# Kernel optimization log

Measured on AMD Instinct MI355X. Metric: run time of the kernel, lower is better.

The kernel has to match this reference:

```python
import jax, jax.numpy as jnp
import numpy as np

B, S, D, H, E = 4, 2048, 1024, 4096, 8
THRESHOLD = 0.5


def setup_inputs() -> dict:
    key = jax.random.key(0)
    ks = jax.random.split(key, 7)
    s_in = 1.0 / np.sqrt(D)
    s_h = 1.0 / np.sqrt(H)
    return {
        "x": jax.random.normal(ks[0], (B, S, D), dtype=jnp.float32),
        "Wg": jax.random.uniform(ks[1], (D, E), jnp.float32, -s_in, s_in),
        "bg": jax.random.uniform(ks[2], (E,), jnp.float32, -s_in, s_in),
        "W1": jax.random.uniform(ks[3], (E, D, H), jnp.float32, -s_in, s_in),
        "b1": jax.random.uniform(ks[4], (E, H), jnp.float32, -s_in, s_in),
        "W2": jax.random.uniform(ks[5], (E, H, D), jnp.float32, -s_h, s_h),
        "b2": jax.random.uniform(ks[6], (E, D), jnp.float32, -s_h, s_h),
    }


def reference(x, Wg, bg, W1, b1, W2, b2):
    b, s, d = x.shape
    x_flat = x.reshape(-1, d)                       # [T, D], T = B*S
    # Top-any gating: sigmoid logits, threshold mask, weights = probs * mask
    probs = jax.nn.sigmoid(x_flat @ Wg + bg)        # [T, E]
    mask = (probs > THRESHOLD).astype(x_flat.dtype)
    weights = probs * mask                          # [T, E]
    # Dense per-expert MLP over all tokens (faithful to the torch loop)
    h = jax.nn.relu(jnp.einsum('td,edh->eth', x_flat, W1) + b1[:, None, :])  # [E, T, H]
    expert_out = jnp.einsum('eth,ehd->etd', h, W2) + b2[:, None, :]          # [E, T, D]
    combined = jnp.einsum('te,etd->td', weights, expert_out)                 # [T, D]
    return combined.reshape(b, s, d)
```

## Files before the change

### kernel.cpp

```cpp
#include <hip/hip_runtime.h>
#include <hip/hip_bf16.h>

#define T_TOK 8192
#define D_DIM 1024
#define H_DIM 4096
#define E_NUM 8
#define IDXST 8448
#define CAPBLK 18
#define CAPROWS (CAPBLK * 256)

typedef short bf16x8 __attribute__((ext_vector_type(8)));
typedef float f32x4 __attribute__((ext_vector_type(4)));

__device__ __forceinline__ unsigned short f2bf(float f) {
    union { float f; unsigned int u; } v; v.f = f;
    unsigned int u = v.u;
    u = u + 0x7FFFu + ((u >> 16) & 1u);
    return (unsigned short)(u >> 16);
}

__device__ __forceinline__ void gload_lds16(const void* g, void* l) {
    __builtin_amdgcn_global_load_lds(
        (const __attribute__((address_space(1))) unsigned int*)g,
        (__attribute__((address_space(3))) unsigned int*)l,
        16, 0, 0);
}

#define SBAR() { __builtin_amdgcn_sched_barrier(0); __builtin_amdgcn_s_barrier(); __builtin_amdgcn_sched_barrier(0); }
#define LGKM0() { asm volatile("s_waitcnt lgkmcnt(0)" ::: "memory"); __builtin_amdgcn_sched_barrier(0); }
#define VMC4() { asm volatile("s_waitcnt vmcnt(4)" ::: "memory"); __builtin_amdgcn_sched_barrier(0); }
#define VMC6() { asm volatile("s_waitcnt vmcnt(6)" ::: "memory"); __builtin_amdgcn_sched_barrier(0); }
#define VMC0() { asm volatile("s_waitcnt vmcnt(0)" ::: "memory"); __builtin_amdgcn_sched_barrier(0); }

__device__ __forceinline__ void swz_bmbn(int lin, int nbm, int nbn, int& bm, int& bn) {
    const int nwg = nbm * nbn;
    int wgid = ((nwg & 7) == 0) ? ((lin & 7) * (nwg >> 3) + (lin >> 3)) : lin;
    if ((nbm & 7) == 0 && (nbn & 3) == 0) {
        const int per = nbn << 3;
        int stripe = wgid / per;
        int l = wgid - stripe * per;
        int g = l >> 5, r = l & 31;
        bm = stripe * 8 + (r >> 2);
        bn = g * 4 + (r & 3);
    } else {
        bm = wgid / nbn;
        bn = wgid - bm * nbn;
    }
}

__device__ __forceinline__ int swz_rt(int lin, int n) {
    int q = n >> 3, r = n & 7;
    int xcd = lin & 7, pos = lin >> 3;
    int base = (xcd < r) ? xcd * (q + 1) : r * (q + 1) + (xcd - r) * q;
    return base + pos;
}

template<int NBN>
__device__ __forceinline__ bool merged_map(const int* __restrict__ cntp,
                                           int& e, int& bm, int& bn, int& cnt_e) {
    int nbs[E_NUM], tot = 0;
    #pragma unroll
    for (int i = 0; i < E_NUM; ++i) {
        int c = cntp[i];
        int nbm = (c + 255) >> 8;
        if (nbm > CAPBLK) nbm = CAPBLK;
        nbs[i] = nbm * NBN;
        tot += nbs[i];
    }
    if ((int)blockIdx.x >= tot) return false;
    const int wg = swz_rt(blockIdx.x, tot);
    int acc = 0, loc = 0;
    e = 0;
    #pragma unroll
    for (int i = 0; i < E_NUM; ++i) {
        if (wg >= acc && wg < acc + nbs[i]) { e = i; loc = wg - acc; }
        acc += nbs[i];
    }
    bm = loc / NBN;
    bn = loc - bm * NBN;
    cnt_e = cntp[e];
    return true;
}

__global__ void gate_cvt_kernel(const float* __restrict__ x, const float* __restrict__ Wg,
                                const float* __restrict__ bg, float* __restrict__ wout,
                                unsigned short* __restrict__ xb) {
    int wv = (int)((blockIdx.x * blockDim.x + threadIdx.x) >> 6);
    int lane = threadIdx.x & 63;
    if (wv >= T_TOK) return;
    const float* xr = x + (size_t)wv * D_DIM;
    unsigned short* xo = xb + (size_t)wv * D_DIM;
    double acc[E_NUM] = {0, 0, 0, 0, 0, 0, 0, 0};
    for (int i = 0; i < D_DIM / 64; ++i) {
        int d = i * 64 + lane;
        float xf = xr[d];
        xo[d] = f2bf(xf);
        double xv = (double)xf;
        const float* wr = Wg + (size_t)d * E_NUM;
        #pragma unroll
        for (int e = 0; e < E_NUM; ++e) acc[e] += xv * (double)wr[e];
    }
    #pragma unroll
    for (int e = 0; e < E_NUM; ++e) {
        double v = acc[e];
        for (int s = 32; s; s >>= 1) v += __shfl_down(v, s, 64);
        acc[e] = v;
    }
    if (lane == 0) {
        #pragma unroll
        for (int e = 0; e < E_NUM; ++e) {
            double z = acc[e] + (double)bg[e];
            float p = (float)(1.0 / (1.0 + exp(-z)));
            wout[(size_t)wv * E_NUM + e] = (p > 0.5f) ? p : 0.0f;
        }
    }
}

__global__ void compact_kernel(const float* __restrict__ wgt, int* __restrict__ idx,
                               float* __restrict__ wc, int* __restrict__ cnt) {
    const int e = blockIdx.x;
    const int tid = threadIdx.x;
    const int lane = tid & 63, wv = tid >> 6;
    int* idxe = idx + e * IDXST;
    float* wce = wc + e * IDXST;
    __shared__ int wtot[4];
    __shared__ int sbase;
    if (tid == 0) sbase = 0;
    __syncthreads();
    for (int t0 = 0; t0 < T_TOK; t0 += 256) {
        int t = t0 + tid;
        float w = wgt[(size_t)t * E_NUM + e];
        int act = (w > 0.0f) ? 1 : 0;
        unsigned long long mask = __ballot(act);
        int wpos = __popcll(mask & ((1ull << lane) - 1ull));
        if (lane == 0) wtot[wv] = __popcll(mask);
        __syncthreads();
        int off = sbase;
        for (int i = 0; i < wv; ++i) off += wtot[i];
        if (act) { idxe[off + wpos] = t; wce[off + wpos] = w; }
        __syncthreads();
        if (tid == 0) sbase += wtot[0] + wtot[1] + wtot[2] + wtot[3];
        __syncthreads();
    }
    int total = sbase;
    int padded = ((total + 255) / 256) * 256;
    for (int i = total + tid; i < padded; i += 256) { idxe[i] = 0; wce[i] = 0.0f; }
    if (tid == 0) cnt[e] = total;
}

__global__ void transpose_cvt(const float* __restrict__ in, unsigned short* __restrict__ out,
                              int R, int C) {
    __shared__ unsigned short tile[64][65];
    int e = blockIdx.z;
    const float* src = in + (size_t)e * R * C;
    unsigned short* dst = out + (size_t)e * R * C;
    int c0 = blockIdx.x * 64, r0 = blockIdx.y * 64;
    int t = threadIdx.x;
    int cc = (t & 15) * 4;
    int rr = t >> 4;
    #pragma unroll
    for (int p = 0; p < 4; ++p) {
        int r = rr + p * 16;
        float4 v = *(const float4*)(src + (size_t)(r0 + r) * C + c0 + cc);
        tile[cc + 0][r] = f2bf(v.x);
        tile[cc + 1][r] = f2bf(v.y);
        tile[cc + 2][r] = f2bf(v.z);
        tile[cc + 3][r] = f2bf(v.w);
    }
    __syncthreads();
    int rr4 = (t & 15) * 4;
    int cw = t >> 4;
    #pragma unroll
    for (int p = 0; p < 4; ++p) {
        int c = cw + p * 16;
        ushort4 o;
        o.x = tile[c][rr4 + 0];
        o.y = tile[c][rr4 + 1];
        o.z = tile[c][rr4 + 2];
        o.w = tile[c][rr4 + 3];
        *(ushort4*)(dst + (size_t)(c0 + c) * R + r0 + rr4) = o;
    }
}

__global__ void zero_kernel(float4* __restrict__ p, size_t n4) {
    size_t i = (size_t)blockIdx.x * blockDim.x + threadIdx.x;
    size_t st = (size_t)gridDim.x * blockDim.x;
    for (; i < n4; i += st) p[i] = (float4){0.f, 0.f, 0.f, 0.f};
}

__global__ void sentinel_kernel(float* out, size_t n) {
    size_t i = (size_t)blockIdx.x * blockDim.x + threadIdx.x;
    size_t st = (size_t)gridDim.x * blockDim.x;
    for (; i < n; i += st) out[i] = 12345.0f;
}

__global__ __launch_bounds__(512, 2) void gemm1c(
    const unsigned short* __restrict__ Xb,
    const unsigned short* __restrict__ W1T,
    unsigned short* __restrict__ Hc,
    const float* __restrict__ b1,
    const int* __restrict__ idxb,
    const float* __restrict__ wcb,
    const int* __restrict__ cntp)
{
    __shared__ __align__(16) unsigned short lA[2][16384];
    __shared__ __align__(16) unsigned short lB[2][16384];

    int e, bm, bn, cnt;
    if (!merged_map<H_DIM / 256>(cntp, e, bm, bn, cnt)) return;

    const int* idx = idxb + e * IDXST;
    const float* wc = wcb + e * IDXST;
    const unsigned short* Bmat = W1T + (size_t)e * H_DIM * D_DIM;
    const float* b1e = b1 + (size_t)e * H_DIM;
    unsigned short* HcE = Hc + (size_t)e * CAPROWS * H_DIM;

    const int tid = threadIdx.x;
    const int lane = tid & 63, wid = tid >> 6;
    const int wr = wid >> 2;
    const int wcn = wid & 3;
    const int fr = lane & 15, fq = lane >> 4;

    const int srow = tid >> 3;
    const int scol = (((tid & 7) ^ (srow & 7)) << 3);

    const unsigned short* Asrc[4];
    #pragma unroll
    for (int h = 0; h < 4; ++h)
        Asrc[h] = Xb + (size_t)idx[bm * 256 + h * 64 + srow] * D_DIM + scol;
    const unsigned short* Bb = Bmat + (size_t)(bn * 256 + srow) * D_DIM + scol;

    const int s0 = ((0 << 2) | fq) ^ (fr & 7);
    const int s1 = ((1 << 2) | fq) ^ (fr & 7);

    f32x4 acc[8][4];
    #pragma unroll
    for (int m = 0; m < 8; ++m)
        #pragma unroll
        for (int n = 0; n < 4; ++n)
            acc[m][n] = (f32x4){0.f, 0.f, 0.f, 0.f};

    bf16x8 a[4][2], b[4][2];

    auto stageA = [&](int bf, int hf, int kt) {
        gload_lds16(Asrc[hf * 2]     + kt * 64, &lA[bf][hf * 8192 + tid * 8]);
        gload_lds16(Asrc[hf * 2 + 1] + kt * 64, &lA[bf][hf * 8192 + 4096 + tid * 8]);
    };
    auto stageB = [&](int bf, int hf, int kt) {
        const unsigned short* s = Bb + (size_t)(hf * 128) * D_DIM + kt * 64;
        gload_lds16(s,                      &lB[bf][hf * 8192 + tid * 8]);
        gload_lds16(s + (size_t)64 * D_DIM, &lB[bf][hf * 8192 + 4096 + tid * 8]);
    };

    stageB(0, 0, 0);
    stageA(0, 0, 0);
    stageA(0, 1, 0);
    stageB(0, 1, 0);
    stageB(1, 0, 1);
    stageA(1, 0, 1);
    VMC4();
    SBAR();

    int cur = 0;
    for (int t = 0; t < 16; ++t) {
        const int nxt = cur ^ 1;
        #pragma unroll
        for (int mm = 0; mm < 4; ++mm) {
            const int r = wr * 128 + mm * 16 + fr;
            a[mm][0] = *(const bf16x8*)&lA[cur][r * 64 + s0 * 8];
            a[mm][1] = *(const bf16x8*)&lA[cur][r * 64 + s1 * 8];
        }
        #pragma unroll
        for (int n = 0; n < 2; ++n) {
            const int r = wcn * 64 + n * 16 + fr;
            b[n][0] = *(const bf16x8*)&lB[cur][r * 64 + s0 * 8];
            b[n][1] = *(const bf16x8*)&lB[cur][r * 64 + s1 * 8];
        }
        if (t + 1 < 16) stageA(nxt, 1, t + 1);
        SBAR(); LGKM0();
        __builtin_amdgcn_s_setprio(1);
        #pragma unroll
        for (int kk = 0; kk < 2; ++kk)
            #pragma unroll
            for (int mm = 0; mm < 4; ++mm) {
                acc[mm][0] = __builtin_amdgcn_mfma_f32_16x16x32_bf16(a[mm][kk], b[0][kk], acc[mm][0], 0, 0, 0);
                acc[mm][1] = __builtin_amdgcn_mfma_f32_16x16x32_bf16(a[mm][kk], b[1][kk], acc[mm][1], 0, 0, 0);
            }
        __builtin_amdgcn_s_setprio(0);
        SBAR();
        #pragma unroll
        for (int n = 2; n < 4; ++n) {
            const int r = wcn * 64 + n * 16 + fr;
            b[n][0] = *(const bf16x8*)&lB[cur][r * 64 + s0 * 8];
            b[n][1] = *(const bf16x8*)&lB[cur][r * 64 + s1 * 8];
        }
        if (t + 1 < 16) stageB(nxt, 1, t + 1);
        SBAR(); LGKM0();
        __builtin_amdgcn_s_setprio(1);
        #pragma unroll
        for (int kk = 0; kk < 2; ++kk)
            #pragma unroll
            for (int mm = 0; mm < 4; ++mm) {
                acc[mm][2] = __builtin_amdgcn_mfma_f32_16x16x32_bf16(a[mm][kk], b[2][kk], acc[mm][2], 0, 0, 0);
                acc[mm][3] = __builtin_amdgcn_mfma_f32_16x16x32_bf16(a[mm][kk], b[3][kk], acc[mm][3], 0, 0, 0);
            }
        __builtin_amdgcn_s_setprio(0);
        SBAR();
        #pragma unroll
        for (int mm = 0; mm < 4; ++mm) {
            const int r = wr * 128 + (mm + 4) * 16 + fr;
            a[mm][0] = *(const bf16x8*)&lA[cur][r * 64 + s0 * 8];
            a[mm][1] = *(const bf16x8*)&lA[cur][r * 64 + s1 * 8];
        }
        if (t + 2 < 16) stageB(cur, 0, t + 2);
        SBAR(); LGKM0();
        __builtin_amdgcn_s_setprio(1);
        #pragma unroll
        for (int kk = 0; kk < 2; ++kk)
            #pragma unroll
            for (int mm = 0; mm < 4; ++mm) {
                acc[mm + 4][0] = __builtin_amdgcn_mfma_f32_16x16x32_bf16(a[mm][kk], b[0][kk], acc[mm + 4][0], 0, 0, 0);
                acc[mm + 4][1] = __builtin_amdgcn_mfma_f32_16x16x32_bf16(a[mm][kk], b[1][kk], acc[mm + 4][1], 0, 0, 0);
            }
        __builtin_amdgcn_s_setprio(0);
        SBAR();
        if (t + 2 < 16) stageA(cur, 0, t + 2);
        if (t < 14) { VMC4(); } else { VMC0(); }
        SBAR(); LGKM0();
        __builtin_amdgcn_s_setprio(1);
        #pragma unroll
        for (int kk = 0; kk < 2; ++kk)
            #pragma unroll
            for (int mm = 0; mm < 4; ++mm) {
                acc[mm + 4][2] = __builtin_amdgcn_mfma_f32_16x16x32_bf16(a[mm][kk], b[2][kk], acc[mm + 4][2], 0, 0, 0);
                acc[mm + 4][3] = __builtin_amdgcn_mfma_f32_16x16x32_bf16(a[mm][kk], b[3][kk], acc[mm + 4][3], 0, 0, 0);
            }
        __builtin_amdgcn_s_setprio(0);
        SBAR();
        cur = nxt;
    }

    #pragma unroll
    for (int m = 0; m < 8; ++m) {
        const int rbase = bm * 256 + wr * 128 + m * 16 + fq * 4;
        #pragma unroll
        for (int n = 0; n < 4; ++n) {
            const int cn = bn * 256 + wcn * 64 + n * 16 + fr;
            const float bb = b1e[cn];
            #pragma unroll
            for (int j = 0; j < 4; ++j) {
                const int r = rbase + j;
                const float w = wc[r];
                float v = fmaxf(acc[m][n][j] + bb, 0.0f) * w;
                HcE[(size_t)r * H_DIM + cn] = f2bf(v);
            }
        }
    }
}

__global__ __launch_bounds__(512, 2) void gemm2c(
    const unsigned short* __restrict__ Hc,
    const unsigned short* __restrict__ W2T,
    float* __restrict__ out,
    const float* __restrict__ b2,
    const int* __restrict__ idxb,
    const float* __restrict__ wcb,
    const int* __restrict__ cntp)
{
    __shared__ __align__(16) unsigned short lA[3][16384];
    __shared__ __align__(16) unsigned short lB[3][8192];

    int e, bm, bn, cnt;
    if (!merged_map<D_DIM / 128>(cntp, e, bm, bn, cnt)) return;

    const int* idx = idxb + e * IDXST;
    const float* wc = wcb + e * IDXST;
    const unsigned short* A = Hc + (size_t)e * CAPROWS * H_DIM;
    const unsigned short* Bmat = W2T + (size_t)e * D_DIM * H_DIM;
    const float* b2e = b2 + (size_t)e * D_DIM;

    const int tid = threadIdx.x;
    const int lane = tid & 63, wid = tid >> 6;
    const int wr = wid >> 1;
    const int wcn = wid & 1;
    const int fr = lane & 15, fq = lane >> 4;

    const int srow = tid >> 3;
    const int scol = (((tid & 7) ^ (srow & 7)) << 3);
    const unsigned short* Ab = A + (size_t)(bm * 256 + srow) * H_DIM + scol;
    const unsigned short* Bb = Bmat + (size_t)(bn * 128 + srow) * H_DIM + scol;

    const int s0 = ((0 << 2) | fq) ^ (fr & 7);
    const int s1 = ((1 << 2) | fq) ^ (fr & 7);

    f32x4 acc[4][4];
    #pragma unroll
    for (int m = 0; m < 4; ++m)
        #pragma unroll
        for (int n = 0; n < 4; ++n)
            acc[m][n] = (f32x4){0.f, 0.f, 0.f, 0.f};

    bf16x8 a[4][2], b[4][2];

    auto stageA = [&](int bf, int hf, int kt) {
        const unsigned short* s = Ab + (size_t)(hf * 128) * H_DIM + kt * 64;
        gload_lds16(s,                      &lA[bf][hf * 8192 + tid * 8]);
        gload_lds16(s + (size_t)64 * H_DIM, &lA[bf][hf * 8192 + 4096 + tid * 8]);
    };
    auto stageB = [&](int bf, int kt) {
        const unsigned short* s = Bb + kt * 64;
        gload_lds16(s,                      &lB[bf][tid * 8]);
        gload_lds16(s + (size_t)64 * H_DIM, &lB[bf][4096 + tid * 8]);
    };

    stageA(0, 0, 0); stageA(0, 1, 0); stageB(0, 0);
    stageA(1, 0, 1); stageA(1, 1, 1); stageB(1, 1);
    VMC6();
    SBAR();

    int bt = 0, bs = 2;
    const int NT = H_DIM / 64;
    for (int t = 0; t < NT; ++t) {
        #pragma unroll
        for (int mm = 0; mm < 4; ++mm) {
            const int r = wr * 64 + mm * 16 + fr;
            a[mm][0] = *(const bf16x8*)&lA[bt][r * 64 + s0 * 8];
            a[mm][1] = *(const bf16x8*)&lA[bt][r * 64 + s1 * 8];
        }
        #pragma unroll
        for (int n = 0; n < 2; ++n) {
            const int r = wcn * 64 + n * 16 + fr;
            b[n][0] = *(const bf16x8*)&lB[bt][r * 64 + s0 * 8];
            b[n][1] = *(const bf16x8*)&lB[bt][r * 64 + s1 * 8];
        }
        if (t + 2 < NT) { stageA(bs, 1, t + 2); stageB(bs, t + 2); }
        SBAR(); LGKM0();
        __builtin_amdgcn_s_setprio(1);
        #pragma unroll
        for (int kk = 0; kk < 2; ++kk)
            #pragma unroll
            for (int mm = 0; mm < 4; ++mm) {
                acc[mm][0] = __builtin_amdgcn_mfma_f32_16x16x32_bf16(a[mm][kk], b[0][kk], acc[mm][0], 0, 0, 0);
                acc[mm][1] = __builtin_amdgcn_mfma_f32_16x16x32_bf16(a[mm][kk], b[1][kk], acc[mm][1], 0, 0, 0);
            }
        __builtin_amdgcn_s_setprio(0);
        SBAR();
        #pragma unroll
        for (int n = 2; n < 4; ++n) {
            const int r = wcn * 64 + n * 16 + fr;
            b[n][0] = *(const bf16x8*)&lB[bt][r * 64 + s0 * 8];
            b[n][1] = *(const bf16x8*)&lB[bt][r * 64 + s1 * 8];
        }
        if (t + 2 < NT) { stageA(bs, 0, t + 2); VMC6(); } else { VMC0(); }
        SBAR(); LGKM0();
        __builtin_amdgcn_s_setprio(1);
        #pragma unroll
        for (int kk = 0; kk < 2; ++kk)
            #pragma unroll
            for (int mm = 0; mm < 4; ++mm) {
                acc[mm][2] = __builtin_amdgcn_mfma_f32_16x16x32_bf16(a[mm][kk], b[2][kk], acc[mm][2], 0, 0, 0);
                acc[mm][3] = __builtin_amdgcn_mfma_f32_16x16x32_bf16(a[mm][kk], b[3][kk], acc[mm][3], 0, 0, 0);
            }
        __builtin_amdgcn_s_setprio(0);
        SBAR();
        bt = (bt == 2) ? 0 : bt + 1;
        bs = (bs == 2) ? 0 : bs + 1;
    }

    #pragma unroll
    for (int m = 0; m < 4; ++m) {
        const int rbase = bm * 256 + wr * 64 + m * 16 + fq * 4;
        #pragma unroll
        for (int n = 0; n < 4; ++n) {
            const int cn = bn * 128 + wcn * 64 + n * 16 + fr;
            const float bb = b2e[cn];
            #pragma unroll
            for (int j = 0; j < 4; ++j) {
                const int row = rbase + j;
                if (row < cnt) {
                    const int tok = idx[row];
                    atomicAdd(&out[(size_t)tok * D_DIM + cn], acc[m][n][j] + wc[row] * bb);
                }
            }
        }
    }
}

__global__ __launch_bounds__(512, 2) void gemm1_8ph(
    const unsigned short* __restrict__ A,
    const unsigned short* __restrict__ W1T,
    unsigned short* __restrict__ Hc,
    const float* __restrict__ b1,
    const float* __restrict__ wgt,
    int t0, int e, int nbm)
{
    __shared__ __align__(16) unsigned short lA[2][16384];
    __shared__ __align__(16) unsigned short lB[2][16384];
    const int nbn = H_DIM / 256;
    int bm, bn;
    swz_bmbn(blockIdx.x, nbm, nbn, bm, bn);
    const int tid = threadIdx.x;
    const int lane = tid & 63, wid = tid >> 6;
    const int wr = wid >> 2;
    const int wcn = wid & 3;
    const int fr = lane & 15, fq = lane >> 4;
    const int srow = tid >> 3;
    const int scol = (((tid & 7) ^ (srow & 7)) << 3);
    const unsigned short* Ab = A + (size_t)(bm * 256 + srow) * D_DIM + scol;
    const unsigned short* Bb = W1T + (size_t)e * H_DIM * D_DIM
                             + (size_t)(bn * 256 + srow) * D_DIM + scol;
    const int s0 = ((0 << 2) | fq) ^ (fr & 7);
    const int s1 = ((1 << 2) | fq) ^ (fr & 7);
    f32x4 acc[8][4];
    #pragma unroll
    for (int m = 0; m < 8; ++m)
        #pragma unroll
        for (int n = 0; n < 4; ++n)
            acc[m][n] = (f32x4){0.f, 0.f, 0.f, 0.f};
    bf16x8 a[4][2], b[4][2];
    auto stageA = [&](int bf, int hf, int kt) {
        const unsigned short* s = Ab + (size_t)(hf * 128) * D_DIM + kt * 64;
        gload_lds16(s,                      &lA[bf][hf * 8192 + tid * 8]);
        gload_lds16(s + (size_t)64 * D_DIM, &lA[bf][hf * 8192 + 4096 + tid * 8]);
    };
    auto stageB = [&](int bf, int hf, int kt) {
        const unsigned short* s = Bb + (size_t)(hf * 128) * D_DIM + kt * 64;
        gload_lds16(s,                      &lB[bf][hf * 8192 + tid * 8]);
        gload_lds16(s + (size_t)64 * D_DIM, &lB[bf][hf * 8192 + 4096 + tid * 8]);
    };
    stageB(0, 0, 0); stageA(0, 0, 0); stageA(0, 1, 0); stageB(0, 1, 0);
    stageB(1, 0, 1); stageA(1, 0, 1);
    VMC4();
    SBAR();
    int cur = 0;
    for (int t = 0; t < 16; ++t) {
        const int nxt = cur ^ 1;
        #pragma unroll
        for (int mm = 0; mm < 4; ++mm) {
            const int r = wr * 128 + mm * 16 + fr;
            a[mm][0] = *(const bf16x8*)&lA[cur][r * 64 + s0 * 8];
            a[mm][1] = *(const bf16x8*)&lA[cur][r * 64 + s1 * 8];
        }
        #pragma unroll
        for (int n = 0; n < 2; ++n) {
            const int r = wcn * 64 + n * 16 + fr;
            b[n][0] = *(const bf16x8*)&lB[cur][r * 64 + s0 * 8];
            b[n][1] = *(const bf16x8*)&lB[cur][r * 64 + s1 * 8];
        }
        if (t + 1 < 16) stageA(nxt, 1, t + 1);
        SBAR(); LGKM0();
        __builtin_amdgcn_s_setprio(1);
        #pragma unroll
        for (int kk = 0; kk < 2; ++kk)
            #pragma unroll
            for (int mm = 0; mm < 4; ++mm) {
                acc[mm][0] = __builtin_amdgcn_mfma_f32_16x16x32_bf16(a[mm][kk], b[0][kk], acc[mm][0], 0, 0, 0);
                acc[mm][1] = __builtin_amdgcn_mfma_f32_16x16x32_bf16(a[mm][kk], b[1][kk], acc[mm][1], 0, 0, 0);
            }
        __builtin_amdgcn_s_setprio(0);
        SBAR();
        #pragma unroll
        for (int n = 2; n < 4; ++n) {
            const int r = wcn * 64 + n * 16 + fr;
            b[n][0] = *(const bf16x8*)&lB[cur][r * 64 + s0 * 8];
            b[n][1] = *(const bf16x8*)&lB[cur][r * 64 + s1 * 8];
        }
        if (t + 1 < 16) stageB(nxt, 1, t + 1);
        SBAR(); LGKM0();
        __builtin_amdgcn_s_setprio(1);
        #pragma unroll
        for (int kk = 0; kk < 2; ++kk)
            #pragma unroll
            for (int mm = 0; mm < 4; ++mm) {
                acc[mm][2] = __builtin_amdgcn_mfma_f32_16x16x32_bf16(a[mm][kk], b[2][kk], acc[mm][2], 0, 0, 0);
                acc[mm][3] = __builtin_amdgcn_mfma_f32_16x16x32_bf16(a[mm][kk], b[3][kk], acc[mm][3], 0, 0, 0);
            }
        __builtin_amdgcn_s_setprio(0);
        SBAR();
        #pragma unroll
        for (int mm = 0; mm < 4; ++mm) {
            const int r = wr * 128 + (mm + 4) * 16 + fr;
            a[mm][0] = *(const bf16x8*)&lA[cur][r * 64 + s0 * 8];
            a[mm][1] = *(const bf16x8*)&lA[cur][r * 64 + s1 * 8];
        }
        if (t + 2 < 16) stageB(cur, 0, t + 2);
        SBAR(); LGKM0();
        __builtin_amdgcn_s_setprio(1);
        #pragma unroll
        for (int kk = 0; kk < 2; ++kk)
            #pragma unroll
            for (int mm = 0; mm < 4; ++mm) {
                acc[mm + 4][0] = __builtin_amdgcn_mfma_f32_16x16x32_bf16(a[mm][kk], b[0][kk], acc[mm + 4][0], 0, 0, 0);
                acc[mm + 4][1] = __builtin_amdgcn_mfma_f32_16x16x32_bf16(a[mm][kk], b[1][kk], acc[mm + 4][1], 0, 0, 0);
            }
        __builtin_amdgcn_s_setprio(0);
        SBAR();
        if (t + 2 < 16) stageA(cur, 0, t + 2);
        if (t < 14) { VMC4(); } else { VMC0(); }
        SBAR(); LGKM0();
        __builtin_amdgcn_s_setprio(1);
        #pragma unroll
        for (int kk = 0; kk < 2; ++kk)
            #pragma unroll
            for (int mm = 0; mm < 4; ++mm) {
                acc[mm + 4][2] = __builtin_amdgcn_mfma_f32_16x16x32_bf16(a[mm][kk], b[2][kk], acc[mm + 4][2], 0, 0, 0);
                acc[mm + 4][3] = __builtin_amdgcn_mfma_f32_16x16x32_bf16(a[mm][kk], b[3][kk], acc[mm + 4][3], 0, 0, 0);
            }
        __builtin_amdgcn_s_setprio(0);
        SBAR();
        cur = nxt;
    }
    #pragma unroll
    for (int m = 0; m < 8; ++m) {
        const int rbase = bm * 256 + wr * 128 + m * 16 + fq * 4;
        #pragma unroll
        for (int n = 0; n < 4; ++n) {
            const int cn = bn * 256 + wcn * 64 + n * 16 + fr;
            const float bb = b1[(size_t)e * H_DIM + cn];
            #pragma unroll
            for (int j = 0; j < 4; ++j) {
                const int r = rbase + j;
                const float w = wgt[(size_t)(t0 + r) * E_NUM + e];
                float v = fmaxf(acc[m][n][j] + bb, 0.0f) * w;
                Hc[(size_t)r * H_DIM + cn] = f2bf(v);
            }
        }
    }
}

template<int MODE>
__global__ __launch_bounds__(512, 2) void gemm2_8ph(
    const unsigned short* __restrict__ A,
    const unsigned short* __restrict__ B,
    float* __restrict__ out,
    const float* __restrict__ bias,
    const float* __restrict__ wts,
    int t0, int e, int nbm)
{
    __shared__ __align__(16) unsigned short lA[3][16384];
    __shared__ __align__(16) unsigned short lB[3][8192];
    const int nbn = D_DIM / 128;
    int bm, bn;
    swz_bmbn(blockIdx.x, nbm, nbn, bm, bn);
    const int tid = threadIdx.x;
    const int lane = tid & 63, wid = tid >> 6;
    const int wr = wid >> 1;
    const int wcn = wid & 1;
    const int fr = lane & 15, fq = lane >> 4;
    const int srow = tid >> 3;
    const int scol = (((tid & 7) ^ (srow & 7)) << 3);
    const unsigned short* Ab = A + (size_t)(bm * 256 + srow) * H_DIM + scol;
    const unsigned short* Bb = B + (size_t)(bn * 128 + srow) * H_DIM + scol;
    const int s0 = ((0 << 2) | fq) ^ (fr & 7);
    const int s1 = ((1 << 2) | fq) ^ (fr & 7);
    f32x4 acc[4][4];
    #pragma unroll
    for (int m = 0; m < 4; ++m)
        #pragma unroll
        for (int n = 0; n < 4; ++n)
            acc[m][n] = (f32x4){0.f, 0.f, 0.f, 0.f};
    bf16x8 a[4][2], b[4][2];
    auto stageA = [&](int bf, int hf, int kt) {
        const unsigned short* s = Ab + (size_t)(hf * 128) * H_DIM + kt * 64;
        gload_lds16(s,                      &lA[bf][hf * 8192 + tid * 8]);
        gload_lds16(s + (size_t)64 * H_DIM, &lA[bf][hf * 8192 + 4096 + tid * 8]);
    };
    auto stageB = [&](int bf, int kt) {
        const unsigned short* s = Bb + kt * 64;
        gload_lds16(s,                      &lB[bf][tid * 8]);
        gload_lds16(s + (size_t)64 * H_DIM, &lB[bf][4096 + tid * 8]);
    };
    stageA(0, 0, 0); stageA(0, 1, 0); stageB(0, 0);
    stageA(1, 0, 1); stageA(1, 1, 1); stageB(1, 1);
    VMC6();
    SBAR();
    int bt = 0, bs = 2;
    const int NT = H_DIM / 64;
    for (int t = 0; t < NT; ++t) {
        #pragma unroll
        for (int mm = 0; mm < 4; ++mm) {
            const int r = wr * 64 + mm * 16 + fr;
            a[mm][0] = *(const bf16x8*)&lA[bt][r * 64 + s0 * 8];
            a[mm][1] = *(const bf16x8*)&lA[bt][r * 64 + s1 * 8];
        }
        #pragma unroll
        for (int n = 0; n < 2; ++n) {
            const int r = wcn * 64 + n * 16 + fr;
            b[n][0] = *(const bf16x8*)&lB[bt][r * 64 + s0 * 8];
            b[n][1] = *(const bf16x8*)&lB[bt][r * 64 + s1 * 8];
        }
        if (t + 2 < NT) { stageA(bs, 1, t + 2); stageB(bs, t + 2); }
        SBAR(); LGKM0();
        __builtin_amdgcn_s_setprio(1);
        #pragma unroll
        for (int kk = 0; kk < 2; ++kk)
            #pragma unroll
            for (int mm = 0; mm < 4; ++mm) {
                acc[mm][0] = __builtin_amdgcn_mfma_f32_16x16x32_bf16(a[mm][kk], b[0][kk], acc[mm][0], 0, 0, 0);
                acc[mm][1] = __builtin_amdgcn_mfma_f32_16x16x32_bf16(a[mm][kk], b[1][kk], acc[mm][1], 0, 0, 0);
            }
        __builtin_amdgcn_s_setprio(0);
        SBAR();
        #pragma unroll
        for (int n = 2; n < 4; ++n) {
            const int r = wcn * 64 + n * 16 + fr;
            b[n][0] = *(const bf16x8*)&lB[bt][r * 64 + s0 * 8];
            b[n][1] = *(const bf16x8*)&lB[bt][r * 64 + s1 * 8];
        }
        if (t + 2 < NT) { stageA(bs, 0, t + 2); VMC6(); } else { VMC0(); }
        SBAR(); LGKM0();
        __builtin_amdgcn_s_setprio(1);
        #pragma unroll
        for (int kk = 0; kk < 2; ++kk)
            #pragma unroll
            for (int mm = 0; mm < 4; ++mm) {
                acc[mm][2] = __builtin_amdgcn_mfma_f32_16x16x32_bf16(a[mm][kk], b[2][kk], acc[mm][2], 0, 0, 0);
                acc[mm][3] = __builtin_amdgcn_mfma_f32_16x16x32_bf16(a[mm][kk], b[3][kk], acc[mm][3], 0, 0, 0);
            }
        __builtin_amdgcn_s_setprio(0);
        SBAR();
        bt = (bt == 2) ? 0 : bt + 1;
        bs = (bs == 2) ? 0 : bs + 1;
    }
    #pragma unroll
    for (int m = 0; m < 4; ++m) {
        const int rbase = bm * 256 + wr * 64 + m * 16 + fq * 4;
        #pragma unroll
        for (int n = 0; n < 4; ++n) {
            const int cn = bn * 128 + wcn * 64 + n * 16 + fr;
            const float bb = bias[cn];
            #pragma unroll
            for (int j = 0; j < 4; ++j) {
                const int row = t0 + rbase + j;
                const float w = wts[(size_t)row * E_NUM + e];
                const float v = acc[m][n][j] + w * bb;
                float* p = out + (size_t)row * D_DIM + cn;
                if (MODE == 1) *p = v;
                else *p += v;
            }
        }
    }
}

extern "C" void kernel_launch(void* const* d_in, const int* in_sizes, int n_in,
                              void* d_out, int out_size, void* d_ws, size_t ws_size,
                              hipStream_t stream) {
    const float* x  = (const float*)d_in[0];
    const float* Wg = (const float*)d_in[1];
    const float* bg = (const float*)d_in[2];
    const float* W1 = (const float*)d_in[3];
    const float* b1 = (const float*)d_in[4];
    const float* W2 = (const float*)d_in[5];
    const float* b2 = (const float*)d_in[6];
    float* out = (float*)d_out;
    char* ws = (char*)d_ws;

    const size_t off_w   = 0;
    const size_t off_idx = 262144;
    const size_t off_wcc = 557056;
    const size_t off_cnt = 851968;
    const size_t off_x   = 1048576;
    const size_t off_w1  = off_x + (size_t)T_TOK * D_DIM * 2;
    const size_t off_w2  = off_w1 + (size_t)E_NUM * D_DIM * H_DIM * 2;
    const size_t off_h   = off_w2 + (size_t)E_NUM * D_DIM * H_DIM * 2;
    const size_t cap_h   = (size_t)E_NUM * CAPROWS * H_DIM * 2;
    const size_t min_h   = (size_t)256 * H_DIM * 2;

    if (ws_size < off_h + min_h) {
        sentinel_kernel<<<2048, 256, 0, stream>>>(out, (size_t)T_TOK * D_DIM);
        return;
    }

    float* wgt = (float*)(ws + off_w);
    int* idxb  = (int*)(ws + off_idx);
    float* wcb = (float*)(ws + off_wcc);
    int* cntb  = (int*)(ws + off_cnt);
    unsigned short* Xb  = (unsigned short*)(ws + off_x);
    unsigned short* W1T = (unsigned short*)(ws + off_w1);
    unsigned short* W2T = (unsigned short*)(ws + off_w2);
    unsigned short* Hc  = (unsigned short*)(ws + off_h);

    gate_cvt_kernel<<<T_TOK / 4, 256, 0, stream>>>(x, Wg, bg, wgt, Xb);
    transpose_cvt<<<dim3(H_DIM / 64, D_DIM / 64, E_NUM), 256, 0, stream>>>(W1, W1T, D_DIM, H_DIM);
    transpose_cvt<<<dim3(D_DIM / 64, H_DIM / 64, E_NUM), 256, 0, stream>>>(W2, W2T, H_DIM, D_DIM);

    if (ws_size >= off_h + cap_h) {
        compact_kernel<<<E_NUM, 256, 0, stream>>>(wgt, idxb, wcb, cntb);
        zero_kernel<<<2048, 256, 0, stream>>>((float4*)out, (size_t)T_TOK * D_DIM / 4);
        const int g1 = E_NUM * CAPBLK * (H_DIM / 256);
        const int g2 = E_NUM * CAPBLK * (D_DIM / 128);
        gemm1c<<<g1, 512, 0, stream>>>(Xb, W1T, Hc, b1, idxb, wcb, cntb);
        gemm2c<<<g2, 512, 0, stream>>>(Hc, W2T, out, b2, idxb, wcb, cntb);
    } else {
        size_t avail = ws_size - off_h;
        size_t tc = avail / ((size_t)H_DIM * 2);
        tc = (tc / 256) * 256;
        if (tc > T_TOK) tc = T_TOK;
        const int TC = (int)tc;
        for (int t0 = 0; t0 < T_TOK; t0 += TC) {
            int cs = (T_TOK - t0 < TC) ? (T_TOK - t0) : TC;
            const int nbm = cs / 256;
            for (int e = 0; e < E_NUM; ++e) {
                gemm1_8ph<<<nbm * (H_DIM / 256), 512, 0, stream>>>(
                    Xb + (size_t)t0 * D_DIM, W1T, Hc, b1, wgt, t0, e, nbm);
                if (e == 0)
                    gemm2_8ph<1><<<nbm * (D_DIM / 128), 512, 0, stream>>>(
                        Hc, W2T + (size_t)e * D_DIM * H_DIM, out,
                        b2 + (size_t)e * D_DIM, wgt, t0, e, nbm);
                else
                    gemm2_8ph<2><<<nbm * (D_DIM / 128), 512, 0, stream>>>(
                        Hc, W2T + (size_t)e * D_DIM * H_DIM, out,
                        b2 + (size_t)e * D_DIM, wgt, t0, e, nbm);
            }
        }
    }
}
```

Baseline: 1.055 ms.

## Split compacted expert GEMM pair into two row-block chunks for cache locality

Runs gemm1c then gemm2c twice, each time over half of every expert's capacity row blocks (blocks 0-8, then 9-17), instead of one large launch of each. The intended gain is that the intermediate H activations written by gemm1 for a chunk are more likely to still be in cache when gemm2 reads them. In exchange it adds two extra kernel launches, shrinks each grid, which can leave a wave tail with idle CUs, and reloads the expert weights once per chunk.

```diff
diff --git a/kernel.cpp b/kernel.cpp
--- a/kernel.cpp
+++ b/kernel.cpp
@@ -7,6 +7,7 @@
 #define E_NUM 8
 #define IDXST 8448
 #define CAPBLK 18
+#define CHALF 9
 #define CAPROWS (CAPBLK * 256)
 
 typedef short bf16x8 __attribute__((ext_vector_type(8)));
@@ -56,18 +57,21 @@
 }
 
 template<int NBN>
-__device__ __forceinline__ bool merged_map(const int* __restrict__ cntp,
+__device__ __forceinline__ bool merged_map(const int* __restrict__ cntp, int chunk,
                                            int& e, int& bm, int& bn, int& cnt_e) {
+    const int lo = chunk ? CHALF : 0;
     int nbs[E_NUM], tot = 0;
     #pragma unroll
     for (int i = 0; i < E_NUM; ++i) {
         int c = cntp[i];
         int nbm = (c + 255) >> 8;
         if (nbm > CAPBLK) nbm = CAPBLK;
-        nbs[i] = nbm * NBN;
+        int hi = chunk ? nbm : ((nbm < CHALF) ? nbm : CHALF);
+        int nb = hi - lo;
+        nbs[i] = (nb > 0) ? nb * NBN : 0;
         tot += nbs[i];
     }
-    if ((int)blockIdx.x >= tot) return false;
+    if (tot == 0 || (int)blockIdx.x >= tot) return false;
     const int wg = swz_rt(blockIdx.x, tot);
     int acc = 0, loc = 0;
     e = 0;
@@ -76,8 +80,8 @@
         if (wg >= acc && wg < acc + nbs[i]) { e = i; loc = wg - acc; }
         acc += nbs[i];
     }
-    bm = loc / NBN;
-    bn = loc - bm * NBN;
+    bm = loc / NBN + lo;
+    bn = loc - (loc / NBN) * NBN;
     cnt_e = cntp[e];
     return true;
 }
@@ -201,13 +205,14 @@
     const float* __restrict__ b1,
     const int* __restrict__ idxb,
     const float* __restrict__ wcb,
-    const int* __restrict__ cntp)
+    const int* __restrict__ cntp,
+    int chunk)
 {
     __shared__ __align__(16) unsigned short lA[2][16384];
     __shared__ __align__(16) unsigned short lB[2][16384];
 
     int e, bm, bn, cnt;
-    if (!merged_map<H_DIM / 256>(cntp, e, bm, bn, cnt)) return;
+    if (!merged_map<H_DIM / 256>(cntp, chunk, e, bm, bn, cnt)) return;
 
     const int* idx = idxb + e * IDXST;
     const float* wc = wcb + e * IDXST;
@@ -365,13 +370,14 @@
     const float* __restrict__ b2,
     const int* __restrict__ idxb,
     const float* __restrict__ wcb,
-    const int* __restrict__ cntp)
+    const int* __restrict__ cntp,
+    int chunk)
 {
     __shared__ __align__(16) unsigned short lA[3][16384];
     __shared__ __align__(16) unsigned short lB[3][8192];
 
     int e, bm, bn, cnt;
-    if (!merged_map<D_DIM / 128>(cntp, e, bm, bn, cnt)) return;
+    if (!merged_map<D_DIM / 128>(cntp, chunk, e, bm, bn, cnt)) return;
 
     const int* idx = idxb + e * IDXST;
     const float* wc = wcb + e * IDXST;
@@ -787,10 +793,12 @@
     if (ws_size >= off_h + cap_h) {
         compact_kernel<<<E_NUM, 256, 0, stream>>>(wgt, idxb, wcb, cntb);
         zero_kernel<<<2048, 256, 0, stream>>>((float4*)out, (size_t)T_TOK * D_DIM / 4);
-        const int g1 = E_NUM * CAPBLK * (H_DIM / 256);
-        const int g2 = E_NUM * CAPBLK * (D_DIM / 128);
-        gemm1c<<<g1, 512, 0, stream>>>(Xb, W1T, Hc, b1, idxb, wcb, cntb);
-        gemm2c<<<g2, 512, 0, stream>>>(Hc, W2T, out, b2, idxb, wcb, cntb);
+        const int g1 = E_NUM * CHALF * (H_DIM / 256);
+        const int g2 = E_NUM * CHALF * (D_DIM / 128);
+        for (int c = 0; c < 2; ++c) {
+            gemm1c<<<g1, 512, 0, stream>>>(Xb, W1T, Hc, b1, idxb, wcb, cntb, c);
+            gemm2c<<<g2, 512, 0, stream>>>(Hc, W2T, out, b2, idxb, wcb, cntb, c);
+        }
     } else {
         size_t avail = ws_size - off_h;
         size_t tc = avail / ((size_t)H_DIM * 2);
```

New measurement: 1.068 ms. Within noise of the previous version (+1.2%).

## Enlarge gemm2c tile to 256x256 with double-buffered 8-phase pipeline

Applied to the files above, without the earlier changes.

Changes the second expert GEMM from 256x128 output tiles with a triple-buffered schedule to 256x256 tiles. It reuses the double-buffered, four-stage MFMA/load interleave already used in gemm1c, with a 2x4 wave layout and 8x4 accumulators per wave. This doubles the reuse of each staged A/B chunk and halves the grid. In exchange it adds accumulator register pressure and gives fewer workgroups, which can leave CUs underfilled when expert token counts are small.

```diff
diff --git a/kernel.cpp b/kernel.cpp
--- a/kernel.cpp
+++ b/kernel.cpp
@@ -29,7 +29,6 @@
 #define SBAR() { __builtin_amdgcn_sched_barrier(0); __builtin_amdgcn_s_barrier(); __builtin_amdgcn_sched_barrier(0); }
 #define LGKM0() { asm volatile("s_waitcnt lgkmcnt(0)" ::: "memory"); __builtin_amdgcn_sched_barrier(0); }
 #define VMC4() { asm volatile("s_waitcnt vmcnt(4)" ::: "memory"); __builtin_amdgcn_sched_barrier(0); }
-#define VMC6() { asm volatile("s_waitcnt vmcnt(6)" ::: "memory"); __builtin_amdgcn_sched_barrier(0); }
 #define VMC0() { asm volatile("s_waitcnt vmcnt(0)" ::: "memory"); __builtin_amdgcn_sched_barrier(0); }
 
 __device__ __forceinline__ void swz_bmbn(int lin, int nbm, int nbn, int& bm, int& bn) {
@@ -262,7 +261,8 @@
     SBAR();
 
     int cur = 0;
-    for (int t = 0; t < 16; ++t) {
+    const int NT = D_DIM / 64;
+    for (int t = 0; t < NT; ++t) {
         const int nxt = cur ^ 1;
         #pragma unroll
         for (int mm = 0; mm < 4; ++mm) {
@@ -276,7 +276,7 @@
             b[n][0] = *(const bf16x8*)&lB[cur][r * 64 + s0 * 8];
             b[n][1] = *(const bf16x8*)&lB[cur][r * 64 + s1 * 8];
         }
-        if (t + 1 < 16) stageA(nxt, 1, t + 1);
+        if (t + 1 < NT) stageA(nxt, 1, t + 1);
         SBAR(); LGKM0();
         __builtin_amdgcn_s_setprio(1);
         #pragma unroll
@@ -294,7 +294,7 @@
             b[n][0] = *(const bf16x8*)&lB[cur][r * 64 + s0 * 8];
             b[n][1] = *(const bf16x8*)&lB[cur][r * 64 + s1 * 8];
         }
-        if (t + 1 < 16) stageB(nxt, 1, t + 1);
+        if (t + 1 < NT) stageB(nxt, 1, t + 1);
         SBAR(); LGKM0();
         __builtin_amdgcn_s_setprio(1);
         #pragma unroll
@@ -312,7 +312,7 @@
             a[mm][0] = *(const bf16x8*)&lA[cur][r * 64 + s0 * 8];
             a[mm][1] = *(const bf16x8*)&lA[cur][r * 64 + s1 * 8];
         }
-        if (t + 2 < 16) stageB(cur, 0, t + 2);
+        if (t + 2 < NT) stageB(cur, 0, t + 2);
         SBAR(); LGKM0();
         __builtin_amdgcn_s_setprio(1);
         #pragma unroll
@@ -324,8 +324,8 @@
             }
         __builtin_amdgcn_s_setprio(0);
         SBAR();
-        if (t + 2 < 16) stageA(cur, 0, t + 2);
-        if (t < 14) { VMC4(); } else { VMC0(); }
+        if (t + 2 < NT) stageA(cur, 0, t + 2);
+        if (t < NT - 2) { VMC4(); } else { VMC0(); }
         SBAR(); LGKM0();
         __builtin_amdgcn_s_setprio(1);
         #pragma unroll
@@ -367,11 +367,11 @@
     const float* __restrict__ wcb,
     const int* __restrict__ cntp)
 {
-    __shared__ __align__(16) unsigned short lA[3][16384];
-    __shared__ __align__(16) unsigned short lB[3][8192];
+    __shared__ __align__(16) unsigned short lA[2][16384];
+    __shared__ __align__(16) unsigned short lB[2][16384];
 
     int e, bm, bn, cnt;
-    if (!merged_map<D_DIM / 128>(cntp, e, bm, bn, cnt)) return;
+    if (!merged_map<D_DIM / 256>(cntp, e, bm, bn, cnt)) return;
 
     const int* idx = idxb + e * IDXST;
     const float* wc = wcb + e * IDXST;
@@ -381,21 +381,21 @@
 
     const int tid = threadIdx.x;
     const int lane = tid & 63, wid = tid >> 6;
-    const int wr = wid >> 1;
-    const int wcn = wid & 1;
+    const int wr = wid >> 2;
+    const int wcn = wid & 3;
     const int fr = lane & 15, fq = lane >> 4;
 
     const int srow = tid >> 3;
     const int scol = (((tid & 7) ^ (srow & 7)) << 3);
     const unsigned short* Ab = A + (size_t)(bm * 256 + srow) * H_DIM + scol;
-    const unsigned short* Bb = Bmat + (size_t)(bn * 128 + srow) * H_DIM + scol;
+    const unsigned short* Bb = Bmat + (size_t)(bn * 256 + srow) * H_DIM + scol;
 
     const int s0 = ((0 << 2) | fq) ^ (fr & 7);
     const int s1 = ((1 << 2) | fq) ^ (fr & 7);
 
-    f32x4 acc[4][4];
-    #pragma unroll
-    for (int m = 0; m < 4; ++m)
+    f32x4 acc[8][4];
+    #pragma unroll
+    for (int m = 0; m < 8; ++m)
         #pragma unroll
         for (int n = 0; n < 4; ++n)
             acc[m][n] = (f32x4){0.f, 0.f, 0.f, 0.f};
@@ -407,33 +407,38 @@
         gload_lds16(s,                      &lA[bf][hf * 8192 + tid * 8]);
         gload_lds16(s + (size_t)64 * H_DIM, &lA[bf][hf * 8192 + 4096 + tid * 8]);
     };
-    auto stageB = [&](int bf, int kt) {
-        const unsigned short* s = Bb + kt * 64;
-        gload_lds16(s,                      &lB[bf][tid * 8]);
-        gload_lds16(s + (size_t)64 * H_DIM, &lB[bf][4096 + tid * 8]);
+    auto stageB = [&](int bf, int hf, int kt) {
+        const unsigned short* s = Bb + (size_t)(hf * 128) * H_DIM + kt * 64;
+        gload_lds16(s,                      &lB[bf][hf * 8192 + tid * 8]);
+        gload_lds16(s + (size_t)64 * H_DIM, &lB[bf][hf * 8192 + 4096 + tid * 8]);
     };
 
-    stageA(0, 0, 0); stageA(0, 1, 0); stageB(0, 0);
-    stageA(1, 0, 1); stageA(1, 1, 1); stageB(1, 1);
-    VMC6();
+    stageB(0, 0, 0);
+    stageA(0, 0, 0);
+    stageA(0, 1, 0);
+    stageB(0, 1, 0);
+    stageB(1, 0, 1);
+    stageA(1, 0, 1);
+    VMC4();
     SBAR();
 
-    int bt = 0, bs = 2;
+    int cur = 0;
     const int NT = H_DIM / 64;
     for (int t = 0; t < NT; ++t) {
+        const int nxt = cur ^ 1;
         #pragma unroll
         for (int mm = 0; mm < 4; ++mm) {
-            const int r = wr * 64 + mm * 16 + fr;
-            a[mm][0] = *(const bf16x8*)&lA[bt][r * 64 + s0 * 8];
-            a[mm][1] = *(const bf16x8*)&lA[bt][r * 64 + s1 * 8];
+            const int r = wr * 128 + mm * 16 + fr;
+            a[mm][0] = *(const bf16x8*)&lA[cur][r * 64 + s0 * 8];
+            a[mm][1] = *(const bf16x8*)&lA[cur][r * 64 + s1 * 8];
         }
         #pragma unroll
         for (int n = 0; n < 2; ++n) {
             const int r = wcn * 64 + n * 16 + fr;
-            b[n][0] = *(const bf16x8*)&lB[bt][r * 64 + s0 * 8];
-            b[n][1] = *(const bf16x8*)&lB[bt][r * 64 + s1 * 8];
-        }
-        if (t + 2 < NT) { stageA(bs, 1, t + 2); stageB(bs, t + 2); }
+            b[n][0] = *(const bf16x8*)&lB[cur][r * 64 + s0 * 8];
+            b[n][1] = *(const bf16x8*)&lB[cur][r * 64 + s1 * 8];
+        }
+        if (t + 1 < NT) stageA(nxt, 1, t + 1);
         SBAR(); LGKM0();
         __builtin_amdgcn_s_setprio(1);
         #pragma unroll
@@ -448,10 +453,10 @@
         #pragma unroll
         for (int n = 2; n < 4; ++n) {
             const int r = wcn * 64 + n * 16 + fr;
-            b[n][0] = *(const bf16x8*)&lB[bt][r * 64 + s0 * 8];
-            b[n][1] = *(const bf16x8*)&lB[bt][r * 64 + s1 * 8];
-        }
-        if (t + 2 < NT) { stageA(bs, 0, t + 2); VMC6(); } else { VMC0(); }
+            b[n][0] = *(const bf16x8*)&lB[cur][r * 64 + s0 * 8];
+            b[n][1] = *(const bf16x8*)&lB[cur][r * 64 + s1 * 8];
+        }
+        if (t + 1 < NT) stageB(nxt, 1, t + 1);
         SBAR(); LGKM0();
         __builtin_amdgcn_s_setprio(1);
         #pragma unroll
@@ -463,16 +468,46 @@
             }
         __builtin_amdgcn_s_setprio(0);
         SBAR();
-        bt = (bt == 2) ? 0 : bt + 1;
-        bs = (bs == 2) ? 0 : bs + 1;
-    }
-
-    #pragma unroll
-    for (int m = 0; m < 4; ++m) {
-        const int rbase = bm * 256 + wr * 64 + m * 16 + fq * 4;
+        #pragma unroll
+        for (int mm = 0; mm < 4; ++mm) {
+            const int r = wr * 128 + (mm + 4) * 16 + fr;
+            a[mm][0] = *(const bf16x8*)&lA[cur][r * 64 + s0 * 8];
+            a[mm][1] = *(const bf16x8*)&lA[cur][r * 64 + s1 * 8];
+        }
+        if (t + 2 < NT) stageB(cur, 0, t + 2);
+        SBAR(); LGKM0();
+        __builtin_amdgcn_s_setprio(1);
+        #pragma unroll
+        for (int kk = 0; kk < 2; ++kk)
+            #pragma unroll
+            for (int mm = 0; mm < 4; ++mm) {
+                acc[mm + 4][0] = __builtin_amdgcn_mfma_f32_16x16x32_bf16(a[mm][kk], b[0][kk], acc[mm + 4][0], 0, 0, 0);
+                acc[mm + 4][1] = __builtin_amdgcn_mfma_f32_16x16x32_bf16(a[mm][kk], b[1][kk], acc[mm + 4][1], 0, 0, 0);
+            }
+        __builtin_amdgcn_s_setprio(0);
+        SBAR();
+        if (t + 2 < NT) stageA(cur, 0, t + 2);
+        if (t < NT - 2) { VMC4(); } else { VMC0(); }
+        SBAR(); LGKM0();
+        __builtin_amdgcn_s_setprio(1);
+        #pragma unroll
+        for (int kk = 0; kk < 2; ++kk)
+            #pragma unroll
+            for (int mm = 0; mm < 4; ++mm) {
+                acc[mm + 4][2] = __builtin_amdgcn_mfma_f32_16x16x32_bf16(a[mm][kk], b[2][kk], acc[mm + 4][2], 0, 0, 0);
+                acc[mm + 4][3] = __builtin_amdgcn_mfma_f32_16x16x32_bf16(a[mm][kk], b[3][kk], acc[mm + 4][3], 0, 0, 0);
+            }
+        __builtin_amdgcn_s_setprio(0);
+        SBAR();
+        cur = nxt;
+    }
+
+    #pragma unroll
+    for (int m = 0; m < 8; ++m) {
+        const int rbase = bm * 256 + wr * 128 + m * 16 + fq * 4;
         #pragma unroll
         for (int n = 0; n < 4; ++n) {
-            const int cn = bn * 128 + wcn * 64 + n * 16 + fr;
+            const int cn = bn * 256 + wcn * 64 + n * 16 + fr;
             const float bb = b2e[cn];
             #pragma unroll
             for (int j = 0; j < 4; ++j) {
@@ -672,7 +707,7 @@
     };
     stageA(0, 0, 0); stageA(0, 1, 0); stageB(0, 0);
     stageA(1, 0, 1); stageA(1, 1, 1); stageB(1, 1);
-    VMC6();
+    asm volatile("s_waitcnt vmcnt(6)" ::: "memory"); __builtin_amdgcn_sched_barrier(0);
     SBAR();
     int bt = 0, bs = 2;
     const int NT = H_DIM / 64;
@@ -707,7 +742,7 @@
             b[n][0] = *(const bf16x8*)&lB[bt][r * 64 + s0 * 8];
             b[n][1] = *(const bf16x8*)&lB[bt][r * 64 + s1 * 8];
         }
-        if (t + 2 < NT) { stageA(bs, 0, t + 2); VMC6(); } else { VMC0(); }
+        if (t + 2 < NT) { stageA(bs, 0, t + 2); asm volatile("s_waitcnt vmcnt(6)" ::: "memory"); __builtin_amdgcn_sched_barrier(0); } else { VMC0(); }
         SBAR(); LGKM0();
         __builtin_amdgcn_s_setprio(1);
         #pragma unroll
@@ -788,7 +823,7 @@
         compact_kernel<<<E_NUM, 256, 0, stream>>>(wgt, idxb, wcb, cntb);
         zero_kernel<<<2048, 256, 0, stream>>>((float4*)out, (size_t)T_TOK * D_DIM / 4);
         const int g1 = E_NUM * CAPBLK * (H_DIM / 256);
-        const int g2 = E_NUM * CAPBLK * (D_DIM / 128);
+        const int g2 = E_NUM * CAPBLK * (D_DIM / 256);
         gemm1c<<<g1, 512, 0, stream>>>(Xb, W1T, Hc, b1, idxb, wcb, cntb);
         gemm2c<<<g2, 512, 0, stream>>>(Hc, W2T, out, b2, idxb, wcb, cntb);
     } else {
```

Measured after the change: 1.044 ms. No clear change (-1.0%).

## Halve gemm2c K-tile to 32 to shrink LDS and raise occupancy

Applied to the files above, without the earlier changes.

The second-GEMM kernel now stages K in steps of 32 instead of 64. This halves its triple-buffered LDS footprint, and the launch bound goes from 2 to 4 workgroups per CU. The inner loop collapses to a single MFMA phase per step with a new XOR swizzle for 32-wide rows, and the wait count is adjusted to match. The aim is more concurrent waves to hide memory latency, at the cost of twice as many barriers and iterations and a tighter register budget that may cause spills.

```diff
diff --git a/kernel.cpp b/kernel.cpp
--- a/kernel.cpp
+++ b/kernel.cpp
@@ -28,8 +28,8 @@
 
 #define SBAR() { __builtin_amdgcn_sched_barrier(0); __builtin_amdgcn_s_barrier(); __builtin_amdgcn_sched_barrier(0); }
 #define LGKM0() { asm volatile("s_waitcnt lgkmcnt(0)" ::: "memory"); __builtin_amdgcn_sched_barrier(0); }
+#define VMC3() { asm volatile("s_waitcnt vmcnt(3)" ::: "memory"); __builtin_amdgcn_sched_barrier(0); }
 #define VMC4() { asm volatile("s_waitcnt vmcnt(4)" ::: "memory"); __builtin_amdgcn_sched_barrier(0); }
-#define VMC6() { asm volatile("s_waitcnt vmcnt(6)" ::: "memory"); __builtin_amdgcn_sched_barrier(0); }
 #define VMC0() { asm volatile("s_waitcnt vmcnt(0)" ::: "memory"); __builtin_amdgcn_sched_barrier(0); }
 
 __device__ __forceinline__ void swz_bmbn(int lin, int nbm, int nbn, int& bm, int& bn) {
@@ -262,7 +262,8 @@
     SBAR();
 
     int cur = 0;
-    for (int t = 0; t < 16; ++t) {
+    const int NT = D_DIM / 64;
+    for (int t = 0; t < NT; ++t) {
         const int nxt = cur ^ 1;
         #pragma unroll
         for (int mm = 0; mm < 4; ++mm) {
@@ -276,7 +277,7 @@
             b[n][0] = *(const bf16x8*)&lB[cur][r * 64 + s0 * 8];
             b[n][1] = *(const bf16x8*)&lB[cur][r * 64 + s1 * 8];
         }
-        if (t + 1 < 16) stageA(nxt, 1, t + 1);
+        if (t + 1 < NT) stageA(nxt, 1, t + 1);
         SBAR(); LGKM0();
         __builtin_amdgcn_s_setprio(1);
         #pragma unroll
@@ -294,7 +295,7 @@
             b[n][0] = *(const bf16x8*)&lB[cur][r * 64 + s0 * 8];
             b[n][1] = *(const bf16x8*)&lB[cur][r * 64 + s1 * 8];
         }
-        if (t + 1 < 16) stageB(nxt, 1, t + 1);
+        if (t + 1 < NT) stageB(nxt, 1, t + 1);
         SBAR(); LGKM0();
         __builtin_amdgcn_s_setprio(1);
         #pragma unroll
@@ -312,7 +313,7 @@
             a[mm][0] = *(const bf16x8*)&lA[cur][r * 64 + s0 * 8];
             a[mm][1] = *(const bf16x8*)&lA[cur][r * 64 + s1 * 8];
         }
-        if (t + 2 < 16) stageB(cur, 0, t + 2);
+        if (t + 2 < NT) stageB(cur, 0, t + 2);
         SBAR(); LGKM0();
         __builtin_amdgcn_s_setprio(1);
         #pragma unroll
@@ -324,8 +325,8 @@
             }
         __builtin_amdgcn_s_setprio(0);
         SBAR();
-        if (t + 2 < 16) stageA(cur, 0, t + 2);
-        if (t < 14) { VMC4(); } else { VMC0(); }
+        if (t + 2 < NT) stageA(cur, 0, t + 2);
+        if (t < NT - 2) { VMC4(); } else { VMC0(); }
         SBAR(); LGKM0();
         __builtin_amdgcn_s_setprio(1);
         #pragma unroll
@@ -358,7 +359,7 @@
     }
 }
 
-__global__ __launch_bounds__(512, 2) void gemm2c(
+__global__ __launch_bounds__(512, 4) void gemm2c(
     const unsigned short* __restrict__ Hc,
     const unsigned short* __restrict__ W2T,
     float* __restrict__ out,
@@ -367,8 +368,8 @@
     const float* __restrict__ wcb,
     const int* __restrict__ cntp)
 {
-    __shared__ __align__(16) unsigned short lA[3][16384];
-    __shared__ __align__(16) unsigned short lB[3][8192];
+    __shared__ __align__(16) unsigned short lA[3][8192];
+    __shared__ __align__(16) unsigned short lB[3][4096];
 
     int e, bm, bn, cnt;
     if (!merged_map<D_DIM / 128>(cntp, e, bm, bn, cnt)) return;
@@ -385,13 +386,12 @@
     const int wcn = wid & 1;
     const int fr = lane & 15, fq = lane >> 4;
 
-    const int srow = tid >> 3;
-    const int scol = (((tid & 7) ^ (srow & 7)) << 3);
+    const int srow = tid >> 2;
+    const int scol = (((tid & 3) ^ ((tid >> 3) & 3)) << 3);
     const unsigned short* Ab = A + (size_t)(bm * 256 + srow) * H_DIM + scol;
     const unsigned short* Bb = Bmat + (size_t)(bn * 128 + srow) * H_DIM + scol;
 
-    const int s0 = ((0 << 2) | fq) ^ (fr & 7);
-    const int s1 = ((1 << 2) | fq) ^ (fr & 7);
+    const int soff = (fq ^ ((fr >> 1) & 3)) * 8;
 
     f32x4 acc[4][4];
     #pragma unroll
@@ -400,71 +400,47 @@
         for (int n = 0; n < 4; ++n)
             acc[m][n] = (f32x4){0.f, 0.f, 0.f, 0.f};
 
-    bf16x8 a[4][2], b[4][2];
-
-    auto stageA = [&](int bf, int hf, int kt) {
-        const unsigned short* s = Ab + (size_t)(hf * 128) * H_DIM + kt * 64;
-        gload_lds16(s,                      &lA[bf][hf * 8192 + tid * 8]);
-        gload_lds16(s + (size_t)64 * H_DIM, &lA[bf][hf * 8192 + 4096 + tid * 8]);
+    bf16x8 a[4], b[4];
+
+    auto stageA = [&](int bf, int kt) {
+        gload_lds16(Ab + kt * 32,                       &lA[bf][tid * 8]);
+        gload_lds16(Ab + (size_t)128 * H_DIM + kt * 32, &lA[bf][4096 + tid * 8]);
     };
     auto stageB = [&](int bf, int kt) {
-        const unsigned short* s = Bb + kt * 64;
-        gload_lds16(s,                      &lB[bf][tid * 8]);
-        gload_lds16(s + (size_t)64 * H_DIM, &lB[bf][4096 + tid * 8]);
+        gload_lds16(Bb + kt * 32, &lB[bf][tid * 8]);
     };
 
-    stageA(0, 0, 0); stageA(0, 1, 0); stageB(0, 0);
-    stageA(1, 0, 1); stageA(1, 1, 1); stageB(1, 1);
-    VMC6();
+    stageA(0, 0); stageB(0, 0);
+    stageA(1, 1); stageB(1, 1);
+    VMC3();
     SBAR();
 
-    int bt = 0, bs = 2;
-    const int NT = H_DIM / 64;
+    const int NT = H_DIM / 32;
+    int cb = 0;
     for (int t = 0; t < NT; ++t) {
+        const int nb2 = (cb + 2 >= 3) ? cb - 1 : cb + 2;
         #pragma unroll
         for (int mm = 0; mm < 4; ++mm) {
             const int r = wr * 64 + mm * 16 + fr;
-            a[mm][0] = *(const bf16x8*)&lA[bt][r * 64 + s0 * 8];
-            a[mm][1] = *(const bf16x8*)&lA[bt][r * 64 + s1 * 8];
-        }
-        #pragma unroll
-        for (int n = 0; n < 2; ++n) {
-            const int r = wcn * 64 + n * 16 + fr;
-            b[n][0] = *(const bf16x8*)&lB[bt][r * 64 + s0 * 8];
-            b[n][1] = *(const bf16x8*)&lB[bt][r * 64 + s1 * 8];
-        }
-        if (t + 2 < NT) { stageA(bs, 1, t + 2); stageB(bs, t + 2); }
-        SBAR(); LGKM0();
-        __builtin_amdgcn_s_setprio(1);
-        #pragma unroll
-        for (int kk = 0; kk < 2; ++kk)
-            #pragma unroll
-            for (int mm = 0; mm < 4; ++mm) {
-                acc[mm][0] = __builtin_amdgcn_mfma_f32_16x16x32_bf16(a[mm][kk], b[0][kk], acc[mm][0], 0, 0, 0);
-                acc[mm][1] = __builtin_amdgcn_mfma_f32_16x16x32_bf16(a[mm][kk], b[1][kk], acc[mm][1], 0, 0, 0);
-            }
-        __builtin_amdgcn_s_setprio(0);
-        SBAR();
-        #pragma unroll
-        for (int n = 2; n < 4; ++n) {
-            const int r = wcn * 64 + n * 16 + fr;
-            b[n][0] = *(const bf16x8*)&lB[bt][r * 64 + s0 * 8];
-            b[n][1] = *(const bf16x8*)&lB[bt][r * 64 + s1 * 8];
-        }
-        if (t + 2 < NT) { stageA(bs, 0, t + 2); VMC6(); } else { VMC0(); }
-        SBAR(); LGKM0();
-        __builtin_amdgcn_s_setprio(1);
-        #pragma unroll
-        for (int kk = 0; kk < 2; ++kk)
-            #pragma unroll
-            for (int mm = 0; mm < 4; ++mm) {
-                acc[mm][2] = __builtin_amdgcn_mfma_f32_16x16x32_bf16(a[mm][kk], b[2][kk], acc[mm][2], 0, 0, 0);
-                acc[mm][3] = __builtin_amdgcn_mfma_f32_16x16x32_bf16(a[mm][kk], b[3][kk], acc[mm][3], 0, 0, 0);
-            }
-        __builtin_amdgcn_s_setprio(0);
-        SBAR();
-        bt = (bt == 2) ? 0 : bt + 1;
-        bs = (bs == 2) ? 0 : bs + 1;
+            a[mm] = *(const bf16x8*)&lA[cb][r * 32 + soff];
+        }
+        #pragma unroll
+        for (int n = 0; n < 4; ++n) {
+            const int rB = wcn * 64 + n * 16 + fr;
+            b[n] = *(const bf16x8*)&lB[cb][rB * 32 + soff];
+        }
+        if (t + 2 < NT) { stageA(nb2, t + 2); stageB(nb2, t + 2); }
+        if (t < NT - 2) { VMC3(); } else { VMC0(); }
+        SBAR(); LGKM0();
+        __builtin_amdgcn_s_setprio(1);
+        #pragma unroll
+        for (int mm = 0; mm < 4; ++mm)
+            #pragma unroll
+            for (int n = 0; n < 4; ++n)
+                acc[mm][n] = __builtin_amdgcn_mfma_f32_16x16x32_bf16(a[mm], b[n], acc[mm][n], 0, 0, 0);
+        __builtin_amdgcn_s_setprio(0);
+        SBAR();
+        cb = (cb == 2) ? 0 : cb + 1;
     }
 
     #pragma unroll
@@ -672,7 +648,7 @@
     };
     stageA(0, 0, 0); stageA(0, 1, 0); stageB(0, 0);
     stageA(1, 0, 1); stageA(1, 1, 1); stageB(1, 1);
-    VMC6();
+    asm volatile("s_waitcnt vmcnt(6)" ::: "memory"); __builtin_amdgcn_sched_barrier(0);
     SBAR();
     int bt = 0, bs = 2;
     const int NT = H_DIM / 64;
@@ -707,7 +683,7 @@
             b[n][0] = *(const bf16x8*)&lB[bt][r * 64 + s0 * 8];
             b[n][1] = *(const bf16x8*)&lB[bt][r * 64 + s1 * 8];
         }
-        if (t + 2 < NT) { stageA(bs, 0, t + 2); VMC6(); } else { VMC0(); }
+        if (t + 2 < NT) { stageA(bs, 0, t + 2); asm volatile("s_waitcnt vmcnt(6)" ::: "memory"); __builtin_amdgcn_sched_barrier(0); } else { VMC0(); }
         SBAR(); LGKM0();
         __builtin_amdgcn_s_setprio(1);
         #pragma unroll
```

After: 925.1 us. -12.3%, faster.
